# Performance work log

Hardware: AMD Instinct MI355X
Metric: run time of the kernel (lower is better)

## Reference

```python
import jax, jax.numpy as jnp
import numpy as np

D_HALF = 255
H = 2 * D_HALF + 1   # 511 channels (2*d+1)
L = 2048             # sequence length
N = 32               # S4D complex state modes per channel
NLAYERS = 4          # l
EPS = 1e-5


def setup_inputs() -> dict:
    key = jax.random.key(0)
    ks = jax.random.split(key, 10)
    Z = jax.random.normal(ks[0], (H, L), dtype=jnp.float32)
    # S4D-Lin initialization
    dt_min, dt_max = 1e-3, 1e-1
    log_dt = (jax.random.uniform(ks[1], (H,), dtype=jnp.float32)
              * (np.log(dt_max) - np.log(dt_min)) + np.log(dt_min))
    A_real_log = jnp.log(0.5 * jnp.ones((H, N), dtype=jnp.float32))
    A_imag = jnp.pi * jnp.broadcast_to(jnp.arange(N, dtype=jnp.float32), (H, N))
    C_re = jax.random.normal(ks[2], (H, N), dtype=jnp.float32)
    C_im = jax.random.normal(ks[3], (H, N), dtype=jnp.float32)
    D_skip = jax.random.normal(ks[4], (H,), dtype=jnp.float32)
    glu_w = jax.random.normal(ks[5], (2 * H, H), dtype=jnp.float32) / np.sqrt(H)
    glu_b = jnp.zeros((2 * H,), dtype=jnp.float32)
    ln_g = jnp.ones((H,), dtype=jnp.float32)
    ln_b = jnp.zeros((H,), dtype=jnp.float32)
    return {"Z": Z, "log_dt": log_dt, "A_real_log": A_real_log, "A_imag": A_imag,
            "C_re": C_re, "C_im": C_im, "D_skip": D_skip,
            "glu_w": glu_w, "glu_b": glu_b, "ln_g": ln_g, "ln_b": ln_b}


def _s4d_kernel(log_dt, A_real_log, A_imag, C_re, C_im):
    # A: (H,N) complex with negative real part; ZOH discretization kernel
    A = -jnp.exp(A_real_log) + 1j * A_imag
    dtA = A * jnp.exp(log_dt)[:, None]                  # (H,N)
    Ccoef = (C_re + 1j * C_im) * (jnp.exp(dtA) - 1.0) / A  # (H,N)
    V = jnp.exp(dtA[:, :, None] * jnp.arange(L, dtype=jnp.float32))  # (H,N,L)
    return 2.0 * jnp.einsum('hn,hnl->hl', Ccoef, V).real  # (H,L)


def _s4_block(Z, K, D_skip, glu_w, glu_b):
    # Z: (B,H,L); causal FFT convolution with kernel K (H,L)
    n = 2 * L
    Kf = jnp.fft.rfft(K, n=n)                  # (H, L+1)
    Uf = jnp.fft.rfft(Z, n=n)                  # (B,H,L+1)
    y = jnp.fft.irfft(Uf * Kf, n=n)[..., :L]   # (B,H,L)
    y = y + D_skip[:, None] * Z
    y = jax.nn.gelu(y)
    # output 1x1 conv H -> 2H followed by GLU over channels
    y2 = jnp.einsum('oh,bhl->bol', glu_w, y) + glu_b[:, None]
    return y2[:, :H] * jax.nn.sigmoid(y2[:, H:])


def _layernorm_channels(Z, g, b):
    # LayerNorm over the channel dim (module does norm(Z.transpose(-1,-2)).transpose(-1,-2))
    zt = jnp.swapaxes(Z, -1, -2)               # (B,L,H)
    mu = jnp.mean(zt, axis=-1, keepdims=True)
    var = jnp.mean((zt - mu) ** 2, axis=-1, keepdims=True)
    zt = (zt - mu) * jax.lax.rsqrt(var + EPS) * g + b
    return jnp.swapaxes(zt, -1, -2)


def reference(Z, log_dt, A_real_log, A_imag, C_re, C_im, D_skip, glu_w, glu_b, ln_g, ln_b):
    K = _s4d_kernel(log_dt, A_real_log, A_imag, C_re, C_im)
    z = Z[None]                                # unsqueeze(0) -> (1,H,L)
    for _ in range(NLAYERS):                   # mode='auto': shared layer, l iterations
        residual = z
        z = _s4_block(z, K, D_skip, glu_w, glu_b)
        z = z + residual
        z = _layernorm_channels(z, ln_g, ln_b)
    return z[0]                                # squeeze(0) -> (H,L)
```

## Files before the change

kernel.cpp:

```cpp
#include <hip/hip_runtime.h>
#include <hip/hip_bf16.h>
#include <math.h>

#define H 511
#define L 2048
#define NST 32
#define NLAYERS 4
#define LN_EPS 1e-5f
#define NCH 32
#define TC (L / NCH)
#define HN (H * NST)
#define HP 512
#define GBK 64
#define GBN 64
#define NSTRIPE 16

typedef __attribute__((ext_vector_type(8))) short short8;
typedef __attribute__((ext_vector_type(4))) float f32x4;

__device__ __forceinline__ ushort f2bf(float v) {
    __hip_bfloat16 b = __float2bfloat16(v);
    return *reinterpret_cast<ushort*>(&b);
}

__global__ __launch_bounds__(256) void pre_kernel(
    const float* __restrict__ log_dt,
    const float* __restrict__ A_real_log,
    const float* __restrict__ A_imag,
    const float* __restrict__ C_re,
    const float* __restrict__ C_im,
    const float* __restrict__ W,
    float* __restrict__ wr_o, float* __restrict__ wi_o,
    float* __restrict__ cr_o, float* __restrict__ ci_o,
    ushort* __restrict__ wbf)
{
    int idx = blockIdx.x * blockDim.x + threadIdx.x;
    if (idx < HN) {
        int h = idx / NST;
        float Ar = -expf(A_real_log[idx]);
        float Ai = A_imag[idx];
        float dt = expf(log_dt[h]);
        float dr = Ar * dt, di = Ai * dt;
        float er = expf(dr);
        float wr = er * cosf(di);
        float wi = er * sinf(di);
        float den = Ar * Ar + Ai * Ai;
        float a = wr - 1.0f, b = wi;
        float inv = 1.0f / den;
        float qr = (a * Ar + b * Ai) * inv;
        float qi = (b * Ar - a * Ai) * inv;
        wr_o[idx] = wr; wi_o[idx] = wi;
        cr_o[idx] = 2.0f * (C_re[idx] * qr - C_im[idx] * qi);
        ci_o[idx] = 2.0f * (C_re[idx] * qi + C_im[idx] * qr);
    }
    if (idx < 2 * H * HP) {
        int r = idx / HP, k = idx % HP;
        float v = (k < H) ? W[(size_t)r * H + k] : 0.0f;
        wbf[idx] = f2bf(v);
    }
}

template <int CTRL, int ROW_MASK>
__device__ __forceinline__ float dpp_add(float x) {
    int r = __builtin_amdgcn_update_dpp(0, __float_as_int(x), CTRL, ROW_MASK, 0xf, true);
    return x + __int_as_float(r);
}
__device__ __forceinline__ float reduce32_to_lane31(float p) {
    p = dpp_add<0x111, 0xf>(p);
    p = dpp_add<0x112, 0xf>(p);
    p = dpp_add<0x114, 0xf>(p);
    p = dpp_add<0x118, 0xf>(p);
    p = dpp_add<0x142, 0xa>(p);
    return p;
}

__device__ __forceinline__ float gelu_tanh(float v) {
    const float c0 = 0.7978845608028654f;
    float t = tanhf(c0 * (v + 0.044715f * v * v * v));
    return 0.5f * v * (1.0f + t);
}

__global__ __launch_bounds__(1024) void conv_fused(
    const float* __restrict__ zsrc,
    const float* __restrict__ psum_p,
    const float* __restrict__ psq_p,
    const float* __restrict__ lng,
    const float* __restrict__ lnb,
    const int donorm,
    const float* __restrict__ wr_,
    const float* __restrict__ wi_,
    const float* __restrict__ cr_,
    const float* __restrict__ ci_,
    const float* __restrict__ D_skip,
    ushort* __restrict__ yb)
{
    __shared__ float zs[L];
    __shared__ float ber[NCH][NST];
    __shared__ float bei[NCH][NST];
    __shared__ float ysf[L];

    const int tid  = threadIdx.x;
    const int wv   = tid >> 6;
    const int half = (tid >> 5) & 1;
    const int ln   = tid & 31;
    const int c    = wv * 2 + half;
    const int h    = blockIdx.x;

    {
        const int c0 = tid * 2;
        float2 v = *(const float2*)&zsrc[(size_t)h * L + c0];
        if (donorm) {
            float2 S = {0.f, 0.f}, Q = {0.f, 0.f};
            #pragma unroll
            for (int k = 0; k < NSTRIPE; ++k) {
                float2 sv = *(const float2*)&psum_p[(size_t)k * L + c0];
                float2 qv = *(const float2*)&psq_p[(size_t)k * L + c0];
                S.x += sv.x; S.y += sv.y;
                Q.x += qv.x; Q.y += qv.y;
            }
            const float invH = 1.0f / (float)H;
            float mu0 = S.x * invH, mu1 = S.y * invH;
            float rs0 = rsqrtf(Q.x * invH - mu0 * mu0 + LN_EPS);
            float rs1 = rsqrtf(Q.y * invH - mu1 * mu1 + LN_EPS);
            float gh = lng[h], bh = lnb[h];
            v.x = (v.x - mu0) * rs0 * gh + bh;
            v.y = (v.y - mu1) * rs1 * gh + bh;
        }
        *(float2*)&zs[tid * 2] = v;
    }

    const int cidx = h * NST + ln;
    const float wr = wr_[cidx], wi = wi_[cidx];
    const float cr = cr_[cidx], ci = ci_[cidx];
    const float Dh = D_skip[h];
    __syncthreads();

    float sr = 0.f, si = 0.f;
    {
        const float* zp = &zs[c * TC];
        #pragma unroll 4
        for (int l = 0; l < TC; ++l) {
            float zl = zp[l];
            float nsr = fmaf(wr, sr, fmaf(-wi, si, zl));
            float nsi = fmaf(wr, si, wi * sr);
            sr = nsr; si = nsi;
        }
    }
    ber[c][ln] = sr;
    bei[c][ln] = si;
    __syncthreads();

    if (tid < 32) {
        float wtr = wr, wti = wi;
        #pragma unroll
        for (int k = 0; k < 6; ++k) {
            float nr = wtr * wtr - wti * wti;
            float ni = 2.0f * wtr * wti;
            wtr = nr; wti = ni;
        }
        float er = 0.f, ei = 0.f;
        #pragma unroll
        for (int cc = 0; cc < NCH; ++cc) {
            float s_r = ber[cc][tid], s_i = bei[cc][tid];
            ber[cc][tid] = er; bei[cc][tid] = ei;
            float ner = fmaf(wtr, er, fmaf(-wti, ei, s_r));
            float nei = fmaf(wtr, ei, fmaf(wti, er, s_i));
            er = ner; ei = nei;
        }
    }
    __syncthreads();

    sr = ber[c][ln];
    si = bei[c][ln];
    {
        const float* zp = &zs[c * TC];
        float* yp = &ysf[c * TC];
        for (int l = 0; l < TC; ++l) {
            float zl = zp[l];
            float nsr = fmaf(wr, sr, fmaf(-wi, si, zl));
            float nsi = fmaf(wr, si, wi * sr);
            sr = nsr; si = nsi;
            float p = fmaf(cr, sr, -ci * si);
            p = reduce32_to_lane31(p);
            if (ln == 31) yp[l] = fmaf(Dh, zl, p);
        }
    }
    __syncthreads();

    {
        ushort2 v;
        v.x = f2bf(gelu_tanh(ysf[tid * 2]));
        v.y = f2bf(gelu_tanh(ysf[tid * 2 + 1]));
        *(ushort2*)&yb[(size_t)h * L + tid * 2] = v;
    }
}

__global__ __launch_bounds__(256) void glu_mfma(
    const ushort* __restrict__ wbf,
    const ushort* __restrict__ yb,
    const float* __restrict__ bias,
    const float* __restrict__ zres,
    const float* __restrict__ psum_p,
    const float* __restrict__ psq_p,
    const float* __restrict__ lng,
    const float* __restrict__ lnb,
    const int donorm,
    float* __restrict__ out,
    float* __restrict__ psum_c,
    float* __restrict__ psq_c)
{
    __shared__ ushort As1[32 * GBK];
    __shared__ ushort As2[32 * GBK];
    __shared__ ushort Bs[GBN * GBK];
    __shared__ ushort tempT[4][32 * 40];
    __shared__ float  sls[2][64];
    __shared__ float  slq[2][64];

    const int tid = threadIdx.x;
    const int h0 = blockIdx.y * 32;
    const int l0 = blockIdx.x * GBN;
    const int wid = tid >> 6;
    const int lane = tid & 63;
    const int wrow = (wid >> 1) * 16;
    const int wcol = (wid & 1) * 32;

    f32x4 acc1[2] = {{0.f,0.f,0.f,0.f},{0.f,0.f,0.f,0.f}};
    f32x4 acc2[2] = {{0.f,0.f,0.f,0.f},{0.f,0.f,0.f,0.f}};

    const int ar = tid >> 3;
    const int ak = tid & 7;
    const int hq1 = (h0 + ar < H) ? (h0 + ar) : (H - 1);
    const int hq2 = hq1 + H;
    const int aswz = ak ^ (ar & 7);

    const int tm   = tid >> 6;
    const int t64  = tid & 63;
    const int ksub = (tm & 1) * 32;
    const int lsub = (tm >> 1) * 32;
    const int bkl  = t64 >> 1;
    const int bhalf= t64 & 1;
    const int blr  = t64 >> 1;
    const int bkh  = t64 & 1;

    for (int k0 = 0; k0 < HP; k0 += GBK) {
        {
            short8 va1 = *(const short8*)&wbf[(size_t)hq1 * HP + k0 + ak * 8];
            short8 va2 = *(const short8*)&wbf[(size_t)hq2 * HP + k0 + ak * 8];
            *(short8*)&As1[ar * GBK + aswz * 8] = va1;
            *(short8*)&As2[ar * GBK + aswz * 8] = va2;
        }
        {
            const int kg = k0 + ksub + bkl;
            short8 v0 = {0,0,0,0,0,0,0,0}, v1 = {0,0,0,0,0,0,0,0};
            if (kg < H) {
                const ushort* row = &yb[(size_t)kg * L + l0 + lsub + bhalf * 16];
                v0 = *(const short8*)&row[0];
                v1 = *(const short8*)&row[8];
            }
            ushort* tp = &tempT[tm][0];
            #pragma unroll
            for (int j = 0; j < 8; ++j)
                tp[(bhalf * 16 + j) * 40 + bkl] = (ushort)v0[j];
            #pragma unroll
            for (int j = 0; j < 8; ++j)
                tp[(bhalf * 16 + 8 + j) * 40 + bkl] = (ushort)v1[j];
        }
        __syncthreads();
        {
            const ushort* tp = &tempT[tm][0];
            short8 b0 = *(const short8*)&tp[blr * 40 + bkh * 16];
            short8 b1 = *(const short8*)&tp[blr * 40 + bkh * 16 + 8];
            const int L_ = lsub + blr;
            const int kg0 = (ksub >> 3) + bkh * 2;
            *(short8*)&Bs[L_ * GBK + ((kg0    ) ^ (L_ & 7)) * 8] = b0;
            *(short8*)&Bs[L_ * GBK + ((kg0 + 1) ^ (L_ & 7)) * 8] = b1;
        }
        __syncthreads();

        #pragma unroll
        for (int kk = 0; kk < 2; ++kk) {
            const int arow = wrow + (lane & 15);
            const int kg = kk * 4 + (lane >> 4);
            short8 a1 = *(const short8*)&As1[arow * GBK + (kg ^ (arow & 7)) * 8];
            short8 a2 = *(const short8*)&As2[arow * GBK + (kg ^ (arow & 7)) * 8];
            #pragma unroll
            for (int nf = 0; nf < 2; ++nf) {
                const int brow = wcol + nf * 16 + (lane & 15);
                short8 b = *(const short8*)&Bs[brow * GBK + (kg ^ (brow & 7)) * 8];
                acc1[nf] = __builtin_amdgcn_mfma_f32_16x16x32_bf16(a1, b, acc1[nf], 0, 0, 0);
                acc2[nf] = __builtin_amdgcn_mfma_f32_16x16x32_bf16(a2, b, acc2[nf], 0, 0, 0);
            }
        }
        __syncthreads();
    }

    float ps[2] = {0.f, 0.f}, pq[2] = {0.f, 0.f};
    #pragma unroll
    for (int nf = 0; nf < 2; ++nf) {
        const int col = l0 + wcol + nf * 16 + (lane & 15);
        float mu = 0.f, rs = 1.f;
        if (donorm) {
            float S = 0.f, Q = 0.f;
            #pragma unroll
            for (int k = 0; k < NSTRIPE; ++k) {
                S += psum_p[(size_t)k * L + col];
                Q += psq_p[(size_t)k * L + col];
            }
            const float invH = 1.0f / (float)H;
            mu = S * invH;
            rs = rsqrtf(Q * invH - mu * mu + LN_EPS);
        }
        #pragma unroll
        for (int r = 0; r < 4; ++r) {
            const int h = h0 + wrow + (lane >> 4) * 4 + r;
            if (h < H) {
                float zv = zres[(size_t)h * L + col];
                if (donorm) zv = (zv - mu) * rs * lng[h] + lnb[h];
                float v1 = acc1[nf][r] + bias[h];
                float v2 = acc2[nf][r] + bias[h + H];
                float o = v1 * (1.0f / (1.0f + expf(-v2))) + zv;
                out[(size_t)h * L + col] = o;
                ps[nf] += o;
                pq[nf] = fmaf(o, o, pq[nf]);
            }
        }
    }
    #pragma unroll
    for (int nf = 0; nf < 2; ++nf) {
        ps[nf] += __shfl_xor(ps[nf], 16, 64);
        ps[nf] += __shfl_xor(ps[nf], 32, 64);
        pq[nf] += __shfl_xor(pq[nf], 16, 64);
        pq[nf] += __shfl_xor(pq[nf], 32, 64);
        if ((lane >> 4) == 0) {
            int cl = wcol + nf * 16 + lane;
            sls[wid >> 1][cl] = ps[nf];
            slq[wid >> 1][cl] = pq[nf];
        }
    }
    __syncthreads();
    if (tid < 64) {
        psum_c[(size_t)blockIdx.y * L + l0 + tid] = sls[0][tid] + sls[1][tid];
        psq_c [(size_t)blockIdx.y * L + l0 + tid] = slq[0][tid] + slq[1][tid];
    }
}

__global__ __launch_bounds__(256) void ln_apply(
    const float* __restrict__ psum, const float* __restrict__ psq,
    const float* __restrict__ g, const float* __restrict__ b,
    float* __restrict__ out)
{
    const int tx = threadIdx.x & 63;
    const int ty = threadIdx.x >> 6;
    const int l = blockIdx.x * 64 + tx;
    const int s = blockIdx.y;

    float S = 0.f, Q = 0.f;
    #pragma unroll
    for (int k = 0; k < NSTRIPE; ++k) {
        S += psum[(size_t)k * L + l];
        Q += psq[(size_t)k * L + l];
    }
    const float invH = 1.0f / (float)H;
    float mu = S * invH;
    float var = Q * invH - mu * mu;
    float rstd = rsqrtf(var + LN_EPS);

    const int hbase = s * 32;
    #pragma unroll
    for (int j = 0; j < 8; ++j) {
        int h = hbase + ty + j * 4;
        if (h < H) {
            float v = out[(size_t)h * L + l];
            out[(size_t)h * L + l] = (v - mu) * rstd * g[h] + b[h];
        }
    }
}

extern "C" void kernel_launch(void* const* d_in, const int* in_sizes, int n_in,
                              void* d_out, int out_size, void* d_ws, size_t ws_size,
                              hipStream_t stream) {
    const float* Z          = (const float*)d_in[0];
    const float* log_dt     = (const float*)d_in[1];
    const float* A_real_log = (const float*)d_in[2];
    const float* A_imag     = (const float*)d_in[3];
    const float* C_re       = (const float*)d_in[4];
    const float* C_im       = (const float*)d_in[5];
    const float* D_skip     = (const float*)d_in[6];
    const float* glu_w      = (const float*)d_in[7];
    const float* glu_b      = (const float*)d_in[8];
    const float* ln_g       = (const float*)d_in[9];
    const float* ln_b       = (const float*)d_in[10];

    float* out = (float*)d_out;
    float* ws  = (float*)d_ws;

    float* wr    = ws;
    float* wi    = wr + HN;
    float* cr    = wi + HN;
    float* ci    = cr + HN;
    float* psumA = ci + HN;
    float* psqA  = psumA + (size_t)NSTRIPE * L;
    float* psumB = psqA + (size_t)NSTRIPE * L;
    float* psqB  = psumB + (size_t)NSTRIPE * L;
    ushort* yb  = (ushort*)(psqB + (size_t)NSTRIPE * L);
    ushort* wbf = yb + (size_t)H * L;

    pre_kernel<<<(2 * H * HP + 255) / 256, 256, 0, stream>>>(
        log_dt, A_real_log, A_imag, C_re, C_im, glu_w,
        wr, wi, cr, ci, wbf);

    const dim3 gg(L / GBN, (H + 31) / 32);
    const dim3 lg(L / 64, NSTRIPE);

    for (int layer = 0; layer < NLAYERS; ++layer) {
        const int donorm = (layer > 0);
        const float* zsrc = (layer == 0) ? Z : out;
        float* psum_c = (layer & 1) ? psumB : psumA;
        float* psq_c  = (layer & 1) ? psqB  : psqA;
        const float* psum_p = (layer & 1) ? psumA : psumB;
        const float* psq_p  = (layer & 1) ? psqA  : psqB;

        conv_fused<<<H, 1024, 0, stream>>>(
            zsrc, psum_p, psq_p, ln_g, ln_b, donorm,
            wr, wi, cr, ci, D_skip, yb);
        glu_mfma<<<gg, 256, 0, stream>>>(
            wbf, yb, glu_b, zsrc, psum_p, psq_p, ln_g, ln_b, donorm,
            out, psum_c, psq_c);
    }
    ln_apply<<<lg, 256, 0, stream>>>(psumB, psqB, ln_g, ln_b, out);
}
```

Before: 238.7 us.

## Fuse all layers into one persistent kernel with software grid barriers

Replaces the prelude, per-layer conv and GLU GEMM launches, and the final layernorm launch with a single persistent kernel of 256 blocks of 1024 threads. Stages are separated by an atomic-counter grid barrier instead of kernel boundaries. Each block now handles two channels in the scan stage, and the GEMM stage runs two 256-thread teams per block while the other half of the threads idle. The B-tile transpose is also simplified to write swizzled LDS directly, dropping one staging pass and a sync. This removes launch overhead but costs occupancy and scan parallelism, since only 256 blocks cover 511 channels sequentially, and the barrier relies on all blocks being co-resident.

```diff
diff --git a/kernel.cpp b/kernel.cpp
--- a/kernel.cpp
+++ b/kernel.cpp
@@ -14,6 +14,7 @@
 #define GBK 64
 #define GBN 64
 #define NSTRIPE 16
+#define NBLK 256
 
 typedef __attribute__((ext_vector_type(8))) short short8;
 typedef __attribute__((ext_vector_type(4))) float f32x4;
@@ -21,43 +22,6 @@
 __device__ __forceinline__ ushort f2bf(float v) {
     __hip_bfloat16 b = __float2bfloat16(v);
     return *reinterpret_cast<ushort*>(&b);
-}
-
-__global__ __launch_bounds__(256) void pre_kernel(
-    const float* __restrict__ log_dt,
-    const float* __restrict__ A_real_log,
-    const float* __restrict__ A_imag,
-    const float* __restrict__ C_re,
-    const float* __restrict__ C_im,
-    const float* __restrict__ W,
-    float* __restrict__ wr_o, float* __restrict__ wi_o,
-    float* __restrict__ cr_o, float* __restrict__ ci_o,
-    ushort* __restrict__ wbf)
-{
-    int idx = blockIdx.x * blockDim.x + threadIdx.x;
-    if (idx < HN) {
-        int h = idx / NST;
-        float Ar = -expf(A_real_log[idx]);
-        float Ai = A_imag[idx];
-        float dt = expf(log_dt[h]);
-        float dr = Ar * dt, di = Ai * dt;
-        float er = expf(dr);
-        float wr = er * cosf(di);
-        float wi = er * sinf(di);
-        float den = Ar * Ar + Ai * Ai;
-        float a = wr - 1.0f, b = wi;
-        float inv = 1.0f / den;
-        float qr = (a * Ar + b * Ai) * inv;
-        float qi = (b * Ar - a * Ai) * inv;
-        wr_o[idx] = wr; wi_o[idx] = wi;
-        cr_o[idx] = 2.0f * (C_re[idx] * qr - C_im[idx] * qi);
-        ci_o[idx] = 2.0f * (C_re[idx] * qi + C_im[idx] * qr);
-    }
-    if (idx < 2 * H * HP) {
-        int r = idx / HP, k = idx % HP;
-        float v = (k < H) ? W[(size_t)r * H + k] : 0.0f;
-        wbf[idx] = f2bf(v);
-    }
 }
 
 template <int CTRL, int ROW_MASK>
@@ -80,298 +44,356 @@
     return 0.5f * v * (1.0f + t);
 }
 
-__global__ __launch_bounds__(1024) void conv_fused(
-    const float* __restrict__ zsrc,
-    const float* __restrict__ psum_p,
-    const float* __restrict__ psq_p,
-    const float* __restrict__ lng,
-    const float* __restrict__ lnb,
-    const int donorm,
-    const float* __restrict__ wr_,
-    const float* __restrict__ wi_,
-    const float* __restrict__ cr_,
-    const float* __restrict__ ci_,
-    const float* __restrict__ D_skip,
-    ushort* __restrict__ yb)
-{
-    __shared__ float zs[L];
-    __shared__ float ber[NCH][NST];
-    __shared__ float bei[NCH][NST];
-    __shared__ float ysf[L];
-
-    const int tid  = threadIdx.x;
-    const int wv   = tid >> 6;
-    const int half = (tid >> 5) & 1;
-    const int ln   = tid & 31;
-    const int c    = wv * 2 + half;
-    const int h    = blockIdx.x;
-
-    {
-        const int c0 = tid * 2;
-        float2 v = *(const float2*)&zsrc[(size_t)h * L + c0];
-        if (donorm) {
-            float2 S = {0.f, 0.f}, Q = {0.f, 0.f};
-            #pragma unroll
-            for (int k = 0; k < NSTRIPE; ++k) {
-                float2 sv = *(const float2*)&psum_p[(size_t)k * L + c0];
-                float2 qv = *(const float2*)&psq_p[(size_t)k * L + c0];
-                S.x += sv.x; S.y += sv.y;
-                Q.x += qv.x; Q.y += qv.y;
-            }
-            const float invH = 1.0f / (float)H;
-            float mu0 = S.x * invH, mu1 = S.y * invH;
-            float rs0 = rsqrtf(Q.x * invH - mu0 * mu0 + LN_EPS);
-            float rs1 = rsqrtf(Q.y * invH - mu1 * mu1 + LN_EPS);
-            float gh = lng[h], bh = lnb[h];
-            v.x = (v.x - mu0) * rs0 * gh + bh;
-            v.y = (v.y - mu1) * rs1 * gh + bh;
-        }
-        *(float2*)&zs[tid * 2] = v;
-    }
-
-    const int cidx = h * NST + ln;
-    const float wr = wr_[cidx], wi = wi_[cidx];
-    const float cr = cr_[cidx], ci = ci_[cidx];
-    const float Dh = D_skip[h];
+__device__ __forceinline__ void grid_barrier(unsigned* cnt, unsigned* gen) {
     __syncthreads();
-
-    float sr = 0.f, si = 0.f;
-    {
-        const float* zp = &zs[c * TC];
-        #pragma unroll 4
-        for (int l = 0; l < TC; ++l) {
-            float zl = zp[l];
-            float nsr = fmaf(wr, sr, fmaf(-wi, si, zl));
-            float nsi = fmaf(wr, si, wi * sr);
-            sr = nsr; si = nsi;
-        }
-    }
-    ber[c][ln] = sr;
-    bei[c][ln] = si;
-    __syncthreads();
-
-    if (tid < 32) {
-        float wtr = wr, wti = wi;
-        #pragma unroll
-        for (int k = 0; k < 6; ++k) {
-            float nr = wtr * wtr - wti * wti;
-            float ni = 2.0f * wtr * wti;
-            wtr = nr; wti = ni;
-        }
-        float er = 0.f, ei = 0.f;
-        #pragma unroll
-        for (int cc = 0; cc < NCH; ++cc) {
-            float s_r = ber[cc][tid], s_i = bei[cc][tid];
-            ber[cc][tid] = er; bei[cc][tid] = ei;
-            float ner = fmaf(wtr, er, fmaf(-wti, ei, s_r));
-            float nei = fmaf(wtr, ei, fmaf(wti, er, s_i));
-            er = ner; ei = nei;
+    if (threadIdx.x == 0) {
+        __threadfence();
+        unsigned g0 = __hip_atomic_load(gen, __ATOMIC_RELAXED, __HIP_MEMORY_SCOPE_AGENT);
+        unsigned arr = __hip_atomic_fetch_add(cnt, 1u, __ATOMIC_ACQ_REL, __HIP_MEMORY_SCOPE_AGENT);
+        if (arr == NBLK - 1u) {
+            __hip_atomic_store(cnt, 0u, __ATOMIC_RELAXED, __HIP_MEMORY_SCOPE_AGENT);
+            __hip_atomic_fetch_add(gen, 1u, __ATOMIC_RELEASE, __HIP_MEMORY_SCOPE_AGENT);
+        } else {
+            while (__hip_atomic_load(gen, __ATOMIC_ACQUIRE, __HIP_MEMORY_SCOPE_AGENT) == g0)
+                __builtin_amdgcn_s_sleep(2);
         }
     }
     __syncthreads();
-
-    sr = ber[c][ln];
-    si = bei[c][ln];
+}
+
+__global__ __launch_bounds__(1024, 4) void s4_mega(
+    const float* __restrict__ Z,
+    const float* __restrict__ log_dt,
+    const float* __restrict__ A_real_log,
+    const float* __restrict__ A_imag,
+    const float* __restrict__ C_re,
+    const float* __restrict__ C_im,
+    const float* __restrict__ D_skip,
+    const float* __restrict__ glu_w,
+    const float* __restrict__ glu_b,
+    const float* __restrict__ ln_g,
+    const float* __restrict__ ln_b,
+    float* __restrict__ out,
+    float* __restrict__ wr_, float* __restrict__ wi_,
+    float* __restrict__ cr_, float* __restrict__ ci_,
+    float* __restrict__ psumA, float* __restrict__ psqA,
+    float* __restrict__ psumB, float* __restrict__ psqB,
+    ushort* __restrict__ yb, ushort* __restrict__ wbf,
+    unsigned* __restrict__ gcnt, unsigned* __restrict__ ggen)
+{
+    __shared__ __align__(16) unsigned char smem[34816];
+    const int tid = threadIdx.x;
+    const int bid = blockIdx.x;
+
+    #pragma unroll
+    for (int ii = 0; ii < 2; ++ii) {
+        int idx = (ii * NBLK + bid) * 1024 + tid;
+        if (idx < HN) {
+            int h = idx / NST;
+            float Ar = -expf(A_real_log[idx]);
+            float Ai = A_imag[idx];
+            float dt = expf(log_dt[h]);
+            float dr = Ar * dt, di = Ai * dt;
+            float er = expf(dr);
+            float wv = er * cosf(di);
+            float wiv = er * sinf(di);
+            float den = Ar * Ar + Ai * Ai;
+            float a = wv - 1.0f, b = wiv;
+            float inv = 1.0f / den;
+            float qr = (a * Ar + b * Ai) * inv;
+            float qi = (b * Ar - a * Ai) * inv;
+            wr_[idx] = wv; wi_[idx] = wiv;
+            cr_[idx] = 2.0f * (C_re[idx] * qr - C_im[idx] * qi);
+            ci_[idx] = 2.0f * (C_re[idx] * qi + C_im[idx] * qr);
+        }
+        if (idx < 2 * H * HP) {
+            int r = idx / HP, k = idx % HP;
+            float v = (k < H) ? glu_w[(size_t)r * H + k] : 0.0f;
+            wbf[idx] = f2bf(v);
+        }
+    }
+    grid_barrier(gcnt, ggen);
+
+    for (int layer = 0; layer < NLAYERS; ++layer) {
+        const int donorm = (layer > 0);
+        const float* zsrc = (layer == 0) ? Z : out;
+        float* psum_c = (layer & 1) ? psumB : psumA;
+        float* psq_c  = (layer & 1) ? psqB  : psqA;
+        const float* psum_p = (layer & 1) ? psumA : psumB;
+        const float* psq_p  = (layer & 1) ? psqA  : psqB;
+
+        {
+            float* zs  = (float*)smem;
+            float* ber = (float*)(smem + 8192);
+            float* bei = (float*)(smem + 12288);
+            float* ysf = (float*)(smem + 16384);
+            const int wv2  = tid >> 6;
+            const int half = (tid >> 5) & 1;
+            const int ln   = tid & 31;
+            const int cch  = wv2 * 2 + half;
+
+            for (int rep = 0; rep < 2; ++rep) {
+                const int ch = bid + rep * NBLK;
+                const bool valid = (ch < H);
+                const int h = valid ? ch : 0;
+
+                {
+                    const int c0 = tid * 2;
+                    float2 v = *(const float2*)&zsrc[(size_t)h * L + c0];
+                    if (donorm) {
+                        float2 S = {0.f, 0.f}, Q = {0.f, 0.f};
+                        #pragma unroll
+                        for (int k = 0; k < NSTRIPE; ++k) {
+                            float2 sv = *(const float2*)&psum_p[(size_t)k * L + c0];
+                            float2 qv = *(const float2*)&psq_p[(size_t)k * L + c0];
+                            S.x += sv.x; S.y += sv.y;
+                            Q.x += qv.x; Q.y += qv.y;
+                        }
+                        const float invH = 1.0f / (float)H;
+                        float mu0 = S.x * invH, mu1 = S.y * invH;
+                        float rs0 = rsqrtf(Q.x * invH - mu0 * mu0 + LN_EPS);
+                        float rs1 = rsqrtf(Q.y * invH - mu1 * mu1 + LN_EPS);
+                        float gh = ln_g[h], bh = ln_b[h];
+                        v.x = (v.x - mu0) * rs0 * gh + bh;
+                        v.y = (v.y - mu1) * rs1 * gh + bh;
+                    }
+                    *(float2*)&zs[tid * 2] = v;
+                }
+                const int cidx = h * NST + ln;
+                const float wrv = wr_[cidx], wiv = wi_[cidx];
+                const float crv = cr_[cidx], civ = ci_[cidx];
+                const float Dh = D_skip[h];
+                __syncthreads();
+
+                float sr = 0.f, si = 0.f;
+                {
+                    const float* zp = &zs[cch * TC];
+                    #pragma unroll 4
+                    for (int l = 0; l < TC; ++l) {
+                        float zl = zp[l];
+                        float nsr = fmaf(wrv, sr, fmaf(-wiv, si, zl));
+                        float nsi = fmaf(wrv, si, wiv * sr);
+                        sr = nsr; si = nsi;
+                    }
+                }
+                ber[cch * NST + ln] = sr;
+                bei[cch * NST + ln] = si;
+                __syncthreads();
+
+                if (tid < 32) {
+                    float wtr = wrv, wti = wiv;
+                    #pragma unroll
+                    for (int k = 0; k < 6; ++k) {
+                        float nr = wtr * wtr - wti * wti;
+                        float ni = 2.0f * wtr * wti;
+                        wtr = nr; wti = ni;
+                    }
+                    float er = 0.f, ei = 0.f;
+                    #pragma unroll
+                    for (int cc = 0; cc < NCH; ++cc) {
+                        float s_r = ber[cc * NST + tid], s_i = bei[cc * NST + tid];
+                        ber[cc * NST + tid] = er; bei[cc * NST + tid] = ei;
+                        float ner = fmaf(wtr, er, fmaf(-wti, ei, s_r));
+                        float nei = fmaf(wtr, ei, fmaf(wti, er, s_i));
+                        er = ner; ei = nei;
+                    }
+                }
+                __syncthreads();
+
+                sr = ber[cch * NST + ln];
+                si = bei[cch * NST + ln];
+                {
+                    const float* zp = &zs[cch * TC];
+                    float* yp = &ysf[cch * TC];
+                    for (int l = 0; l < TC; ++l) {
+                        float zl = zp[l];
+                        float nsr = fmaf(wrv, sr, fmaf(-wiv, si, zl));
+                        float nsi = fmaf(wrv, si, wiv * sr);
+                        sr = nsr; si = nsi;
+                        float p = fmaf(crv, sr, -civ * si);
+                        p = reduce32_to_lane31(p);
+                        if (ln == 31) yp[l] = fmaf(Dh, zl, p);
+                    }
+                }
+                __syncthreads();
+
+                if (valid) {
+                    ushort2 v;
+                    v.x = f2bf(gelu_tanh(ysf[tid * 2]));
+                    v.y = f2bf(gelu_tanh(ysf[tid * 2 + 1]));
+                    *(ushort2*)&yb[(size_t)h * L + tid * 2] = v;
+                }
+                __syncthreads();
+            }
+        }
+        grid_barrier(gcnt, ggen);
+
+        {
+            const int team = tid >> 8;
+            const int t    = tid & 255;
+            const int gt   = bid * 2 + (team & 1);
+            const bool act = (team < 2);
+            unsigned char* base = smem + (team & 1) * 17408;
+            ushort* As1 = (ushort*)base;
+            ushort* As2 = (ushort*)(base + 4096);
+            ushort* Bs  = (ushort*)(base + 8192);
+            float*  sls = (float*)(base + 16384);
+            float*  slq = (float*)(base + 16896);
+
+            const int l0 = (gt & 31) * GBN;
+            const int h0 = (gt >> 5) * 32;
+            const int wid = t >> 6;
+            const int lane = t & 63;
+            const int wrow = (wid >> 1) * 16;
+            const int wcol = (wid & 1) * 32;
+
+            f32x4 acc1[2] = {{0.f,0.f,0.f,0.f},{0.f,0.f,0.f,0.f}};
+            f32x4 acc2[2] = {{0.f,0.f,0.f,0.f},{0.f,0.f,0.f,0.f}};
+
+            const int ar = t >> 3;
+            const int ak = t & 7;
+            const int hq1 = (h0 + ar < H) ? (h0 + ar) : (H - 1);
+            const int hq2 = hq1 + H;
+            const int aswz = ak ^ (ar & 7);
+
+            const int tm    = t >> 6;
+            const int t64   = t & 63;
+            const int ksub  = (tm & 1) * 32;
+            const int lsub  = (tm >> 1) * 32;
+            const int bkl   = t64 >> 1;
+            const int bhalf = t64 & 1;
+            const int kloc  = ksub + bkl;
+            const int oct   = kloc >> 3;
+            const int kin   = kloc & 7;
+
+            for (int k0 = 0; k0 < HP; k0 += GBK) {
+                if (act) {
+                    short8 va1 = *(const short8*)&wbf[(size_t)hq1 * HP + k0 + ak * 8];
+                    short8 va2 = *(const short8*)&wbf[(size_t)hq2 * HP + k0 + ak * 8];
+                    *(short8*)&As1[ar * GBK + aswz * 8] = va1;
+                    *(short8*)&As2[ar * GBK + aswz * 8] = va2;
+
+                    const int kg = k0 + kloc;
+                    short8 v0 = {0,0,0,0,0,0,0,0}, v1 = {0,0,0,0,0,0,0,0};
+                    if (kg < H) {
+                        const ushort* row = &yb[(size_t)kg * L + l0 + lsub + bhalf * 16];
+                        v0 = *(const short8*)&row[0];
+                        v1 = *(const short8*)&row[8];
+                    }
+                    #pragma unroll
+                    for (int j = 0; j < 8; ++j) {
+                        int Lr = lsub + bhalf * 16 + j;
+                        Bs[Lr * GBK + ((oct ^ (Lr & 7)) << 3) + kin] = (ushort)v0[j];
+                    }
+                    #pragma unroll
+                    for (int j = 0; j < 8; ++j) {
+                        int Lr = lsub + bhalf * 16 + 8 + j;
+                        Bs[Lr * GBK + ((oct ^ (Lr & 7)) << 3) + kin] = (ushort)v1[j];
+                    }
+                }
+                __syncthreads();
+                if (act) {
+                    #pragma unroll
+                    for (int kk = 0; kk < 2; ++kk) {
+                        const int arow = wrow + (lane & 15);
+                        const int kg = kk * 4 + (lane >> 4);
+                        short8 a1 = *(const short8*)&As1[arow * GBK + (kg ^ (arow & 7)) * 8];
+                        short8 a2 = *(const short8*)&As2[arow * GBK + (kg ^ (arow & 7)) * 8];
+                        #pragma unroll
+                        for (int nf = 0; nf < 2; ++nf) {
+                            const int brow = wcol + nf * 16 + (lane & 15);
+                            short8 b = *(const short8*)&Bs[brow * GBK + (kg ^ (brow & 7)) * 8];
+                            acc1[nf] = __builtin_amdgcn_mfma_f32_16x16x32_bf16(a1, b, acc1[nf], 0, 0, 0);
+                            acc2[nf] = __builtin_amdgcn_mfma_f32_16x16x32_bf16(a2, b, acc2[nf], 0, 0, 0);
+                        }
+                    }
+                }
+                __syncthreads();
+            }
+
+            float ps[2] = {0.f, 0.f}, pq[2] = {0.f, 0.f};
+            if (act) {
+                #pragma unroll
+                for (int nf = 0; nf < 2; ++nf) {
+                    const int col = l0 + wcol + nf * 16 + (lane & 15);
+                    float mu = 0.f, rs = 1.f;
+                    if (donorm) {
+                        float S = 0.f, Q = 0.f;
+                        #pragma unroll
+                        for (int k = 0; k < NSTRIPE; ++k) {
+                            S += psum_p[(size_t)k * L + col];
+                            Q += psq_p[(size_t)k * L + col];
+                        }
+                        const float invH = 1.0f / (float)H;
+                        mu = S * invH;
+                        rs = rsqrtf(Q * invH - mu * mu + LN_EPS);
+                    }
+                    #pragma unroll
+                    for (int r = 0; r < 4; ++r) {
+                        const int h = h0 + wrow + (lane >> 4) * 4 + r;
+                        if (h < H) {
+                            float zv = zsrc[(size_t)h * L + col];
+                            if (donorm) zv = (zv - mu) * rs * ln_g[h] + ln_b[h];
+                            float v1 = acc1[nf][r] + glu_b[h];
+                            float v2 = acc2[nf][r] + glu_b[h + H];
+                            float o = v1 * (1.0f / (1.0f + expf(-v2))) + zv;
+                            out[(size_t)h * L + col] = o;
+                            ps[nf] += o;
+                            pq[nf] = fmaf(o, o, pq[nf]);
+                        }
+                    }
+                }
+                #pragma unroll
+                for (int nf = 0; nf < 2; ++nf) {
+                    ps[nf] += __shfl_xor(ps[nf], 16, 64);
+                    ps[nf] += __shfl_xor(ps[nf], 32, 64);
+                    pq[nf] += __shfl_xor(pq[nf], 16, 64);
+                    pq[nf] += __shfl_xor(pq[nf], 32, 64);
+                    if ((lane >> 4) == 0) {
+                        int cl = wcol + nf * 16 + lane;
+                        sls[(wid >> 1) * 64 + cl] = ps[nf];
+                        slq[(wid >> 1) * 64 + cl] = pq[nf];
+                    }
+                }
+            }
+            __syncthreads();
+            if (act && t < 64) {
+                psum_c[(size_t)(gt >> 5) * L + l0 + t] = sls[t] + sls[64 + t];
+                psq_c [(size_t)(gt >> 5) * L + l0 + t] = slq[t] + slq[64 + t];
+            }
+        }
+        grid_barrier(gcnt, ggen);
+    }
+
     {
-        const float* zp = &zs[c * TC];
-        float* yp = &ysf[c * TC];
-        for (int l = 0; l < TC; ++l) {
-            float zl = zp[l];
-            float nsr = fmaf(wr, sr, fmaf(-wi, si, zl));
-            float nsi = fmaf(wr, si, wi * sr);
-            sr = nsr; si = nsi;
-            float p = fmaf(cr, sr, -ci * si);
-            p = reduce32_to_lane31(p);
-            if (ln == 31) yp[l] = fmaf(Dh, zl, p);
-        }
-    }
-    __syncthreads();
-
-    {
-        ushort2 v;
-        v.x = f2bf(gelu_tanh(ysf[tid * 2]));
-        v.y = f2bf(gelu_tanh(ysf[tid * 2 + 1]));
-        *(ushort2*)&yb[(size_t)h * L + tid * 2] = v;
-    }
-}
-
-__global__ __launch_bounds__(256) void glu_mfma(
-    const ushort* __restrict__ wbf,
-    const ushort* __restrict__ yb,
-    const float* __restrict__ bias,
-    const float* __restrict__ zres,
-    const float* __restrict__ psum_p,
-    const float* __restrict__ psq_p,
-    const float* __restrict__ lng,
-    const float* __restrict__ lnb,
-    const int donorm,
-    float* __restrict__ out,
-    float* __restrict__ psum_c,
-    float* __restrict__ psq_c)
-{
-    __shared__ ushort As1[32 * GBK];
-    __shared__ ushort As2[32 * GBK];
-    __shared__ ushort Bs[GBN * GBK];
-    __shared__ ushort tempT[4][32 * 40];
-    __shared__ float  sls[2][64];
-    __shared__ float  slq[2][64];
-
-    const int tid = threadIdx.x;
-    const int h0 = blockIdx.y * 32;
-    const int l0 = blockIdx.x * GBN;
-    const int wid = tid >> 6;
-    const int lane = tid & 63;
-    const int wrow = (wid >> 1) * 16;
-    const int wcol = (wid & 1) * 32;
-
-    f32x4 acc1[2] = {{0.f,0.f,0.f,0.f},{0.f,0.f,0.f,0.f}};
-    f32x4 acc2[2] = {{0.f,0.f,0.f,0.f},{0.f,0.f,0.f,0.f}};
-
-    const int ar = tid >> 3;
-    const int ak = tid & 7;
-    const int hq1 = (h0 + ar < H) ? (h0 + ar) : (H - 1);
-    const int hq2 = hq1 + H;
-    const int aswz = ak ^ (ar & 7);
-
-    const int tm   = tid >> 6;
-    const int t64  = tid & 63;
-    const int ksub = (tm & 1) * 32;
-    const int lsub = (tm >> 1) * 32;
-    const int bkl  = t64 >> 1;
-    const int bhalf= t64 & 1;
-    const int blr  = t64 >> 1;
-    const int bkh  = t64 & 1;
-
-    for (int k0 = 0; k0 < HP; k0 += GBK) {
-        {
-            short8 va1 = *(const short8*)&wbf[(size_t)hq1 * HP + k0 + ak * 8];
-            short8 va2 = *(const short8*)&wbf[(size_t)hq2 * HP + k0 + ak * 8];
-            *(short8*)&As1[ar * GBK + aswz * 8] = va1;
-            *(short8*)&As2[ar * GBK + aswz * 8] = va2;
-        }
-        {
-            const int kg = k0 + ksub + bkl;
-            short8 v0 = {0,0,0,0,0,0,0,0}, v1 = {0,0,0,0,0,0,0,0};
-            if (kg < H) {
-                const ushort* row = &yb[(size_t)kg * L + l0 + lsub + bhalf * 16];
-                v0 = *(const short8*)&row[0];
-                v1 = *(const short8*)&row[8];
-            }
-            ushort* tp = &tempT[tm][0];
-            #pragma unroll
-            for (int j = 0; j < 8; ++j)
-                tp[(bhalf * 16 + j) * 40 + bkl] = (ushort)v0[j];
-            #pragma unroll
-            for (int j = 0; j < 8; ++j)
-                tp[(bhalf * 16 + 8 + j) * 40 + bkl] = (ushort)v1[j];
-        }
-        __syncthreads();
-        {
-            const ushort* tp = &tempT[tm][0];
-            short8 b0 = *(const short8*)&tp[blr * 40 + bkh * 16];
-            short8 b1 = *(const short8*)&tp[blr * 40 + bkh * 16 + 8];
-            const int L_ = lsub + blr;
-            const int kg0 = (ksub >> 3) + bkh * 2;
-            *(short8*)&Bs[L_ * GBK + ((kg0    ) ^ (L_ & 7)) * 8] = b0;
-            *(short8*)&Bs[L_ * GBK + ((kg0 + 1) ^ (L_ & 7)) * 8] = b1;
-        }
-        __syncthreads();
-
-        #pragma unroll
-        for (int kk = 0; kk < 2; ++kk) {
-            const int arow = wrow + (lane & 15);
-            const int kg = kk * 4 + (lane >> 4);
-            short8 a1 = *(const short8*)&As1[arow * GBK + (kg ^ (arow & 7)) * 8];
-            short8 a2 = *(const short8*)&As2[arow * GBK + (kg ^ (arow & 7)) * 8];
-            #pragma unroll
-            for (int nf = 0; nf < 2; ++nf) {
-                const int brow = wcol + nf * 16 + (lane & 15);
-                short8 b = *(const short8*)&Bs[brow * GBK + (kg ^ (brow & 7)) * 8];
-                acc1[nf] = __builtin_amdgcn_mfma_f32_16x16x32_bf16(a1, b, acc1[nf], 0, 0, 0);
-                acc2[nf] = __builtin_amdgcn_mfma_f32_16x16x32_bf16(a2, b, acc2[nf], 0, 0, 0);
-            }
-        }
-        __syncthreads();
-    }
-
-    float ps[2] = {0.f, 0.f}, pq[2] = {0.f, 0.f};
-    #pragma unroll
-    for (int nf = 0; nf < 2; ++nf) {
-        const int col = l0 + wcol + nf * 16 + (lane & 15);
-        float mu = 0.f, rs = 1.f;
-        if (donorm) {
+        const int team = tid >> 8;
+        const int t = tid & 255;
+        if (team < 2) {
+            const int gt = bid * 2 + team;
+            const int tx = t & 63;
+            const int ty = t >> 6;
+            const int l = (gt & 31) * 64 + tx;
+            const int s = gt >> 5;
+
             float S = 0.f, Q = 0.f;
             #pragma unroll
             for (int k = 0; k < NSTRIPE; ++k) {
-                S += psum_p[(size_t)k * L + col];
-                Q += psq_p[(size_t)k * L + col];
+                S += psumB[(size_t)k * L + l];
+                Q += psqB[(size_t)k * L + l];
             }
             const float invH = 1.0f / (float)H;
-            mu = S * invH;
-            rs = rsqrtf(Q * invH - mu * mu + LN_EPS);
-        }
-        #pragma unroll
-        for (int r = 0; r < 4; ++r) {
-            const int h = h0 + wrow + (lane >> 4) * 4 + r;
-            if (h < H) {
-                float zv = zres[(size_t)h * L + col];
-                if (donorm) zv = (zv - mu) * rs * lng[h] + lnb[h];
-                float v1 = acc1[nf][r] + bias[h];
-                float v2 = acc2[nf][r] + bias[h + H];
-                float o = v1 * (1.0f / (1.0f + expf(-v2))) + zv;
-                out[(size_t)h * L + col] = o;
-                ps[nf] += o;
-                pq[nf] = fmaf(o, o, pq[nf]);
-            }
-        }
-    }
-    #pragma unroll
-    for (int nf = 0; nf < 2; ++nf) {
-        ps[nf] += __shfl_xor(ps[nf], 16, 64);
-        ps[nf] += __shfl_xor(ps[nf], 32, 64);
-        pq[nf] += __shfl_xor(pq[nf], 16, 64);
-        pq[nf] += __shfl_xor(pq[nf], 32, 64);
-        if ((lane >> 4) == 0) {
-            int cl = wcol + nf * 16 + lane;
-            sls[wid >> 1][cl] = ps[nf];
-            slq[wid >> 1][cl] = pq[nf];
-        }
-    }
-    __syncthreads();
-    if (tid < 64) {
-        psum_c[(size_t)blockIdx.y * L + l0 + tid] = sls[0][tid] + sls[1][tid];
-        psq_c [(size_t)blockIdx.y * L + l0 + tid] = slq[0][tid] + slq[1][tid];
-    }
-}
-
-__global__ __launch_bounds__(256) void ln_apply(
-    const float* __restrict__ psum, const float* __restrict__ psq,
-    const float* __restrict__ g, const float* __restrict__ b,
-    float* __restrict__ out)
-{
-    const int tx = threadIdx.x & 63;
-    const int ty = threadIdx.x >> 6;
-    const int l = blockIdx.x * 64 + tx;
-    const int s = blockIdx.y;
-
-    float S = 0.f, Q = 0.f;
-    #pragma unroll
-    for (int k = 0; k < NSTRIPE; ++k) {
-        S += psum[(size_t)k * L + l];
-        Q += psq[(size_t)k * L + l];
-    }
-    const float invH = 1.0f / (float)H;
-    float mu = S * invH;
-    float var = Q * invH - mu * mu;
-    float rstd = rsqrtf(var + LN_EPS);
-
-    const int hbase = s * 32;
-    #pragma unroll
-    for (int j = 0; j < 8; ++j) {
-        int h = hbase + ty + j * 4;
-        if (h < H) {
-            float v = out[(size_t)h * L + l];
-            out[(size_t)h * L + l] = (v - mu) * rstd * g[h] + b[h];
+            float mu = S * invH;
+            float rstd = rsqrtf(Q * invH - mu * mu + LN_EPS);
+
+            const int hbase = s * 32;
+            #pragma unroll
+            for (int j = 0; j < 8; ++j) {
+                int h = hbase + ty + j * 4;
+                if (h < H) {
+                    float v = out[(size_t)h * L + l];
+                    out[(size_t)h * L + l] = (v - mu) * rstd * ln_g[h] + ln_b[h];
+                }
+            }
         }
     }
 }
@@ -394,7 +416,10 @@
     float* out = (float*)d_out;
     float* ws  = (float*)d_ws;
 
-    float* wr    = ws;
+    unsigned* gcnt = (unsigned*)ws;
+    unsigned* ggen = gcnt + 1;
+    float* base  = ws + 64;
+    float* wr    = base;
     float* wi    = wr + HN;
     float* cr    = wi + HN;
     float* ci    = cr + HN;
@@ -405,27 +430,11 @@
     ushort* yb  = (ushort*)(psqB + (size_t)NSTRIPE * L);
     ushort* wbf = yb + (size_t)H * L;
 
-    pre_kernel<<<(2 * H * HP + 255) / 256, 256, 0, stream>>>(
-        log_dt, A_real_log, A_imag, C_re, C_im, glu_w,
-        wr, wi, cr, ci, wbf);
-
-    const dim3 gg(L / GBN, (H + 31) / 32);
-    const dim3 lg(L / 64, NSTRIPE);
-
-    for (int layer = 0; layer < NLAYERS; ++layer) {
-        const int donorm = (layer > 0);
-        const float* zsrc = (layer == 0) ? Z : out;
-        float* psum_c = (layer & 1) ? psumB : psumA;
-        float* psq_c  = (layer & 1) ? psqB  : psqA;
-        const float* psum_p = (layer & 1) ? psumA : psumB;
-        const float* psq_p  = (layer & 1) ? psqA  : psqB;
-
-        conv_fused<<<H, 1024, 0, stream>>>(
-            zsrc, psum_p, psq_p, ln_g, ln_b, donorm,
-            wr, wi, cr, ci, D_skip, yb);
-        glu_mfma<<<gg, 256, 0, stream>>>(
-            wbf, yb, glu_b, zsrc, psum_p, psq_p, ln_g, ln_b, donorm,
-            out, psum_c, psq_c);
-    }
-    ln_apply<<<lg, 256, 0, stream>>>(psumB, psqB, ln_g, ln_b, out);
-}
+    hipMemsetAsync(d_ws, 0, 256, stream);
+
+    s4_mega<<<NBLK, 1024, 0, stream>>>(
+        Z, log_dt, A_real_log, A_imag, C_re, C_im, D_skip,
+        glu_w, glu_b, ln_g, ln_b, out,
+        wr, wi, cr, ci, psumA, psqA, psumB, psqB,
+        yb, wbf, gcnt, ggen);
+}
```

Result: slower. 582.4 us (+144.0%).
